# Optimization experiments

Measured on AMD Instinct MI355X. Metric: run time of the kernel, lower is better.

The kernel has to match this reference:

```python
import jax, jax.numpy as jnp
import numpy as np

N_NODES = 100000
N_EDGES = 800000
VOCAB = 100
D_FEAT = 10
D = 64
EPS = 1e-8  # torch F.cosine_similarity eps


def setup_inputs() -> dict:
    key = jax.random.key(0)
    ks = jax.random.split(key, 8)
    return {
        "nodes": jax.random.randint(ks[0], (N_NODES,), 0, VOCAB),
        "edges": jax.random.randint(ks[1], (N_EDGES, 2), 0, N_NODES),
        "features": jax.random.normal(ks[2], (N_NODES, D_FEAT), dtype=jnp.float32),
        "node_emb": jax.random.normal(ks[3], (VOCAB, D), dtype=jnp.float32),
        "feat_W": jax.random.normal(ks[4], (D, D_FEAT), dtype=jnp.float32) * 0.1,
        "feat_b": jnp.zeros((D,), dtype=jnp.float32),
        "conv1_W": jax.random.normal(ks[5], (D, D), dtype=jnp.float32) * 0.1,
        "conv1_b": jnp.zeros((D,), dtype=jnp.float32),
        "pattern_emb": jax.random.normal(ks[6], (VOCAB, D), dtype=jnp.float32),
        "pattern_id": 42,  # hash(node_type) % 100
    }


def reference(nodes, edges, features, node_emb, feat_W, feat_b,
              conv1_W, conv1_b, pattern_emb, pattern_id):
    # initial embeddings: type embedding + linear feature projection  [N, D]
    embeds = node_emb[nodes] + (features @ feat_W.T + feat_b)

    src, dst = edges[:, 0], edges[:, 1]
    for _ in range(2):  # fixed 2 message-passing rounds (structural loop)
        # scatter-add messages from src to dst (order-independent sum)
        agg = jnp.zeros_like(embeds).at[dst].add(embeds[src])
        embeds = jax.nn.relu((embeds + agg) @ conv1_W.T + conv1_b)

    # cosine similarity of each node embedding against the pattern embedding
    p = pattern_emb[pattern_id]  # [D]
    num = embeds @ p  # [N]
    denom = jnp.maximum(jnp.linalg.norm(embeds, axis=1), EPS) * \
            jnp.maximum(jnp.linalg.norm(p), EPS)
    return num / denom  # [N] match scores
```

## Files before the change

### kernel.cpp

```cpp
#include <hip/hip_runtime.h>
#include <hip/hip_bf16.h>

#define N_NODES 100000
#define N_EDGES 800000
#define D 64
#define SCAN_B 256
#define NB1 ((N_NODES + SCAN_B - 1) / SCAN_B)
#define FILL_BLOCKS (N_EDGES / 256)
#define INIT_BLOCKS (N_NODES * D / 256)
#define CT 64
#define XS 68
#define OS 72

__device__ __forceinline__ unsigned short f2bf(float f) {
    union { float f; unsigned u; } v; v.f = f;
    unsigned r = v.u + 0x7fffu + ((v.u >> 16) & 1u);
    return (unsigned short)(r >> 16);
}
__device__ __forceinline__ void acc_bf8(float acc[8], uint4 u) {
    acc[0] += __uint_as_float(u.x << 16);
    acc[1] += __uint_as_float(u.x & 0xffff0000u);
    acc[2] += __uint_as_float(u.y << 16);
    acc[3] += __uint_as_float(u.y & 0xffff0000u);
    acc[4] += __uint_as_float(u.z << 16);
    acc[5] += __uint_as_float(u.z & 0xffff0000u);
    acc[6] += __uint_as_float(u.w << 16);
    acc[7] += __uint_as_float(u.w & 0xffff0000u);
}

__global__ __launch_bounds__(256) void hist_rank_kernel(
        const int2* __restrict__ edges,
        int* __restrict__ deg,
        int* __restrict__ rank) {
    int t = blockIdx.x * 256 + threadIdx.x;
    int2 e = edges[t];
    rank[t] = atomicAdd(&deg[e.y], 1);
}

__global__ void scan1_kernel(const int* __restrict__ deg,
                             int* __restrict__ row_ptr,
                             int* __restrict__ bsum) {
    __shared__ int tmp[SCAN_B];
    int t = threadIdx.x;
    int i = blockIdx.x * SCAN_B + t;
    int v = (i < N_NODES) ? deg[i] : 0;
    tmp[t] = v;
    __syncthreads();
#pragma unroll
    for (int off = 1; off < SCAN_B; off <<= 1) {
        int a = (t >= off) ? tmp[t - off] : 0;
        __syncthreads();
        tmp[t] += a;
        __syncthreads();
    }
    if (i < N_NODES) row_ptr[i] = tmp[t] - v;
    if (t == SCAN_B - 1) bsum[blockIdx.x] = tmp[t];
}

__global__ void scan2_kernel(const int* __restrict__ bsum, int* __restrict__ boff) {
    __shared__ int tmp[512];
    int t = threadIdx.x;
    int v = (t < NB1) ? bsum[t] : 0;
    tmp[t] = v;
    __syncthreads();
#pragma unroll
    for (int off = 1; off < 512; off <<= 1) {
        int a = (t >= off) ? tmp[t - off] : 0;
        __syncthreads();
        tmp[t] += a;
        __syncthreads();
    }
    if (t < NB1) boff[t] = tmp[t] - v;
}

__global__ void scan3_kernel(int* __restrict__ row_ptr,
                             const int* __restrict__ boff) {
    int i = blockIdx.x * SCAN_B + threadIdx.x;
    if (i < N_NODES) row_ptr[i] += boff[i >> 8];
    if (i == 0) row_ptr[N_NODES] = N_EDGES;
}

__global__ __launch_bounds__(256) void fill_init_kernel(
        const int2* __restrict__ edges,
        const int* __restrict__ rank,
        const int* __restrict__ rowp,
        int* __restrict__ col,
        const int* __restrict__ nodes,
        const float* __restrict__ features,
        const float* __restrict__ node_emb,
        const float* __restrict__ feat_W,
        const float* __restrict__ feat_b,
        unsigned short* __restrict__ embeds) {
    if (blockIdx.x < FILL_BLOCKS) {
        int t = blockIdx.x * 256 + threadIdx.x;
        int2 e = edges[t];
        col[rowp[e.y] + rank[t]] = e.x;
    } else {
        int tid = (blockIdx.x - FILL_BLOCKS) * 256 + threadIdx.x;
        int node = tid >> 6;
        int d = tid & 63;
        float acc = feat_b[d];
        const float* f = features + (size_t)node * 10;
        const float* w = feat_W + (size_t)d * 10;
#pragma unroll
        for (int j = 0; j < 10; ++j) acc += f[j] * w[j];
        embeds[tid] = f2bf(node_emb[(size_t)nodes[node] * D + d] + acc);
    }
}

__global__ __launch_bounds__(256, 6) void gather_x_kernel(
        const unsigned short* __restrict__ emb_in,
        const int* __restrict__ rowp,
        const int* __restrict__ col,
        float* __restrict__ x_out) {
    int lane = threadIdx.x & 63;
    int wv   = threadIdx.x >> 6;
    int node = blockIdx.x * 4 + wv;
    int g = lane >> 3;
    int c = lane & 7;

    int start = rowp[node];
    int end   = rowp[node + 1];

    float acc[8];
#pragma unroll
    for (int j = 0; j < 8; ++j) acc[j] = 0.f;
    if (g == 0) {
        uint4 u = ((const uint4*)(emb_in + (size_t)node * D))[c];
        acc_bf8(acc, u);
    }

    for (int base = start; base < end; base += 32) {
        int nb = end - base; if (nb > 32) nb = 32;
        int idx = (lane < nb) ? col[base + lane] : 0;
#pragma unroll
        for (int r = 0; r < 4; ++r) {
            int s = r * 8 + g;
            int src = __shfl(idx, s, 64);
            if (s < nb) {
                uint4 u = ((const uint4*)(emb_in + (size_t)src * D))[c];
                acc_bf8(acc, u);
            }
        }
    }

#pragma unroll
    for (int m = 8; m <= 32; m <<= 1) {
#pragma unroll
        for (int j = 0; j < 8; ++j) acc[j] += __shfl_xor(acc[j], m, 64);
    }

    if (g == 0) {
        float4 a0 = make_float4(acc[0], acc[1], acc[2], acc[3]);
        float4 a1 = make_float4(acc[4], acc[5], acc[6], acc[7]);
        float4* o = (float4*)(x_out + (size_t)node * D);
        o[2 * c]     = a0;
        o[2 * c + 1] = a1;
    }
}

template <bool SCORE>
__global__ __launch_bounds__(256) void conv_tile_kernel(
        const float* __restrict__ x,
        const float* __restrict__ W,
        const float* __restrict__ b,
        const float* __restrict__ pattern_emb,
        const int* __restrict__ pattern_id,
        unsigned short* __restrict__ emb_out,
        float* __restrict__ score_out) {
    __shared__ float Xs[CT][XS];
    __shared__ float Wsh[D][XS];
    __shared__ unsigned short Os[CT][OS];
    __shared__ float ps[D];

    int t = threadIdx.x;
    int base = blockIdx.x * CT;
    int i = t & 15;
    int j = t >> 4;

    float bj[4];
#pragma unroll
    for (int dj = 0; dj < 4; ++dj) bj[dj] = b[j + 16 * dj];

    {
        int c = t & 15;
        int r0 = t >> 4;
#pragma unroll
        for (int p4 = 0; p4 < 4; ++p4) {
            int r = r0 + p4 * 16;
            float4 wv4 = ((const float4*)(W + (size_t)r * D))[c];
            *((float4*)&Wsh[r][4 * c]) = wv4;
            int node = base + r;
            int nc = node < N_NODES ? node : (N_NODES - 1);
            float4 xv4 = ((const float4*)(x + (size_t)nc * D))[c];
            *((float4*)&Xs[r][4 * c]) = xv4;
        }
    }
    if (SCORE && t < D) ps[t] = pattern_emb[(size_t)pattern_id[0] * D + t];
    __syncthreads();

    float acc[4][4] = {};
    for (int k4 = 0; k4 < 16; ++k4) {
        float4 xr[4], wr[4];
#pragma unroll
        for (int di = 0; di < 4; ++di) xr[di] = *((const float4*)&Xs[i + 16 * di][4 * k4]);
#pragma unroll
        for (int dj = 0; dj < 4; ++dj) wr[dj] = *((const float4*)&Wsh[j + 16 * dj][4 * k4]);
#pragma unroll
        for (int di = 0; di < 4; ++di)
#pragma unroll
            for (int dj = 0; dj < 4; ++dj)
                acc[di][dj] += xr[di].x * wr[dj].x + xr[di].y * wr[dj].y
                             + xr[di].z * wr[dj].z + xr[di].w * wr[dj].w;
    }

    if (!SCORE) {
#pragma unroll
        for (int di = 0; di < 4; ++di)
#pragma unroll
            for (int dj = 0; dj < 4; ++dj)
                Os[i + 16 * di][j + 16 * dj] = f2bf(fmaxf(acc[di][dj] + bj[dj], 0.f));
        __syncthreads();
#pragma unroll
        for (int q = 0; q < 2; ++q) {
            int idx = t + q * 256;
            int r = idx >> 3, seg = idx & 7;
            int node = base + r;
            if (node < N_NODES)
                ((uint4*)(emb_out + (size_t)node * D))[seg] = *((const uint4*)&Os[r][8 * seg]);
        }
    } else {
        __syncthreads();
#pragma unroll
        for (int di = 0; di < 4; ++di)
#pragma unroll
            for (int dj = 0; dj < 4; ++dj)
                Xs[i + 16 * di][j + 16 * dj] = fmaxf(acc[di][dj] + bj[dj], 0.f);
        __syncthreads();
        if (t < CT) {
            float dot = 0.f, n2 = 0.f, pn = 0.f;
#pragma unroll 8
            for (int k = 0; k < D; ++k) {
                float yk = Xs[t][k];
                float pk = ps[k];
                dot += yk * pk; n2 += yk * yk; pn += pk * pk;
            }
            int node = base + t;
            if (node < N_NODES)
                score_out[node] = dot / (fmaxf(sqrtf(n2), 1e-8f) * fmaxf(sqrtf(pn), 1e-8f));
        }
    }
}

__global__ void init_embeds_kernel(const int* __restrict__ nodes,
                                   const float* __restrict__ features,
                                   const float* __restrict__ node_emb,
                                   const float* __restrict__ feat_W,
                                   const float* __restrict__ feat_b,
                                   float* __restrict__ embeds) {
    int tid = blockIdx.x * blockDim.x + threadIdx.x;
    if (tid >= N_NODES * D) return;
    int node = tid >> 6;
    int d = tid & 63;
    float acc = feat_b[d];
    const float* f = features + (size_t)node * 10;
    const float* w = feat_W + (size_t)d * 10;
#pragma unroll
    for (int j = 0; j < 10; ++j) acc += f[j] * w[j];
    embeds[tid] = node_emb[(size_t)nodes[node] * D + d] + acc;
}

__global__ void scatter_add_kernel(const int* __restrict__ edges,
                                   const float* __restrict__ embeds,
                                   float* __restrict__ agg) {
    int tid = blockIdx.x * blockDim.x + threadIdx.x;
    int edge = tid >> 6;
    int lane = tid & 63;
    if (edge >= N_EDGES) return;
    int src = edges[2 * edge + 0];
    int dst = edges[2 * edge + 1];
    atomicAdd(&agg[(size_t)dst * D + lane], embeds[(size_t)src * D + lane]);
}

__global__ void conv_inplace_kernel(const float* __restrict__ agg,
                                    const float* __restrict__ W,
                                    const float* __restrict__ b,
                                    float* __restrict__ embeds) {
    __shared__ float Ws[D * 65];
    __shared__ float xs[4][D];
    for (int i = threadIdx.x; i < D * D; i += blockDim.x) {
        int d = i >> 6, k = i & 63;
        Ws[d * 65 + k] = W[i];
    }
    __syncthreads();
    int lane_d = threadIdx.x & 63;
    int local_n = threadIdx.x >> 6;
    float bias = b[lane_d];
    const int n_chunks = (N_NODES + 3) / 4;
    for (int chunk = blockIdx.x; chunk < n_chunks; chunk += gridDim.x) {
        int node = chunk * 4 + local_n;
        if (node < N_NODES) {
            size_t base = (size_t)node * D + lane_d;
            xs[local_n][lane_d] = embeds[base] + agg[base];
        }
        __syncthreads();
        if (node < N_NODES) {
            float acc = bias;
#pragma unroll
            for (int k = 0; k < D; ++k) acc += xs[local_n][k] * Ws[lane_d * 65 + k];
            embeds[(size_t)node * D + lane_d] = fmaxf(acc, 0.0f);
        }
        __syncthreads();
    }
}

__global__ void final_score_kernel(const float* __restrict__ embeds,
                                   const float* __restrict__ pattern_emb,
                                   const int* __restrict__ pattern_id,
                                   float* __restrict__ out) {
    int lane = threadIdx.x & 63;
    int wave = threadIdx.x >> 6;
    int node = blockIdx.x * 4 + wave;
    int pid = pattern_id[0];
    float p = pattern_emb[(size_t)pid * D + lane];
    float pn = p * p;
#pragma unroll
    for (int m = 32; m > 0; m >>= 1) pn += __shfl_xor(pn, m, 64);
    if (node < N_NODES) {
        float e = embeds[(size_t)node * D + lane];
        float dot = e * p;
        float n2 = e * e;
#pragma unroll
        for (int m = 32; m > 0; m >>= 1) {
            dot += __shfl_xor(dot, m, 64);
            n2  += __shfl_xor(n2, m, 64);
        }
        if (lane == 0) {
            float denom = fmaxf(sqrtf(n2), 1e-8f) * fmaxf(sqrtf(pn), 1e-8f);
            out[node] = dot / denom;
        }
    }
}

extern "C" void kernel_launch(void* const* d_in, const int* in_sizes, int n_in,
                              void* d_out, int out_size, void* d_ws, size_t ws_size,
                              hipStream_t stream) {
    const int*   nodes       = (const int*)d_in[0];
    const int*   edges       = (const int*)d_in[1];
    const float* features    = (const float*)d_in[2];
    const float* node_emb    = (const float*)d_in[3];
    const float* feat_W      = (const float*)d_in[4];
    const float* feat_b      = (const float*)d_in[5];
    const float* conv1_W     = (const float*)d_in[6];
    const float* conv1_b     = (const float*)d_in[7];
    const float* pattern_emb = (const float*)d_in[8];
    const int*   pattern_id  = (const int*)d_in[9];
    float* out = (float*)d_out;

    const size_t emb_f32_bytes = (size_t)N_NODES * D * sizeof(float);
    const size_t emb_bf_bytes  = (size_t)N_NODES * D * 2;
    auto align256 = [](size_t x) { return (x + 255) & ~(size_t)255; };

    size_t o_embA = 0;
    size_t o_embB = o_embA + align256(emb_bf_bytes);
    size_t o_xbuf = o_embB + align256(emb_bf_bytes);
    size_t o_col  = o_xbuf + align256(emb_f32_bytes);
    size_t o_rank = o_col  + align256((size_t)N_EDGES * 4);
    size_t o_row  = o_rank + align256((size_t)N_EDGES * 4);
    size_t o_deg  = o_row  + align256((size_t)(N_NODES + 1) * 4);
    size_t o_bsum = o_deg  + align256((size_t)N_NODES * 4);
    size_t o_boff = o_bsum + align256((size_t)NB1 * 4);
    size_t need   = o_boff + align256((size_t)NB1 * 4);

    char* ws = (char*)d_ws;

    if (ws_size >= need) {
        unsigned short* embA = (unsigned short*)(ws + o_embA);
        unsigned short* embB = (unsigned short*)(ws + o_embB);
        float* xbuf = (float*)(ws + o_xbuf);
        int*   col  = (int*)(ws + o_col);
        int*   rank = (int*)(ws + o_rank);
        int*   rowp = (int*)(ws + o_row);
        int*   deg  = (int*)(ws + o_deg);
        int*   bsum = (int*)(ws + o_bsum);
        int*   boff = (int*)(ws + o_boff);

        hipMemsetAsync(deg, 0, (size_t)N_NODES * 4, stream);
        hist_rank_kernel<<<FILL_BLOCKS, 256, 0, stream>>>((const int2*)edges, deg, rank);
        scan1_kernel<<<NB1, SCAN_B, 0, stream>>>(deg, rowp, bsum);
        scan2_kernel<<<1, 512, 0, stream>>>(bsum, boff);
        scan3_kernel<<<NB1, SCAN_B, 0, stream>>>(rowp, boff);
        fill_init_kernel<<<FILL_BLOCKS + INIT_BLOCKS, 256, 0, stream>>>(
            (const int2*)edges, rank, rowp, col,
            nodes, features, node_emb, feat_W, feat_b, embA);

        const int conv_grid = (N_NODES + CT - 1) / CT;

        gather_x_kernel<<<N_NODES / 4, 256, 0, stream>>>(embA, rowp, col, xbuf);
        conv_tile_kernel<false><<<conv_grid, 256, 0, stream>>>(
            xbuf, conv1_W, conv1_b, pattern_emb, pattern_id, embB, nullptr);
        gather_x_kernel<<<N_NODES / 4, 256, 0, stream>>>(embB, rowp, col, xbuf);
        conv_tile_kernel<true><<<conv_grid, 256, 0, stream>>>(
            xbuf, conv1_W, conv1_b, pattern_emb, pattern_id, nullptr, out);
    } else {
        float* embeds = (float*)ws;
        float* agg = (float*)(ws + align256(emb_f32_bytes));
        init_embeds_kernel<<<(N_NODES * D + 255) / 256, 256, 0, stream>>>(
            nodes, features, node_emb, feat_W, feat_b, embeds);
        for (int it = 0; it < 2; ++it) {
            hipMemsetAsync(agg, 0, emb_f32_bytes, stream);
            long long total = (long long)N_EDGES * 64;
            scatter_add_kernel<<<(int)((total + 255) / 256), 256, 0, stream>>>(edges, embeds, agg);
            conv_inplace_kernel<<<2048, 256, 0, stream>>>(agg, conv1_W, conv1_b, embeds);
        }
        final_score_kernel<<<(N_NODES + 3) / 4, 256, 0, stream>>>(
            embeds, pattern_emb, pattern_id, out);
    }
}
```

Before: 259.7 us.

## Merge scan passes and rewrite gather to one wave-wide row per neighbor

Replaces the separate block-sum scan and offset-add kernels with one kernel where each block reduces the preceding block sums itself, removing a launch and a serial single-block step. The gather kernel is rewritten so each of the 64 lanes reads one bf16 element of a neighbor row (128-byte row per wave per neighbor) instead of 8 lanes reading 16-byte chunks for 8 neighbors at once. This drops the cross-lane shuffle reduction and uses two accumulators, but it has fewer bytes in flight per lane and issues more load instructions per neighbor. The launch-bounds occupancy hint is also removed.

```diff
diff --git a/kernel.cpp b/kernel.cpp
--- a/kernel.cpp
+++ b/kernel.cpp
@@ -17,15 +17,8 @@
     unsigned r = v.u + 0x7fffu + ((v.u >> 16) & 1u);
     return (unsigned short)(r >> 16);
 }
-__device__ __forceinline__ void acc_bf8(float acc[8], uint4 u) {
-    acc[0] += __uint_as_float(u.x << 16);
-    acc[1] += __uint_as_float(u.x & 0xffff0000u);
-    acc[2] += __uint_as_float(u.y << 16);
-    acc[3] += __uint_as_float(u.y & 0xffff0000u);
-    acc[4] += __uint_as_float(u.z << 16);
-    acc[5] += __uint_as_float(u.z & 0xffff0000u);
-    acc[6] += __uint_as_float(u.w << 16);
-    acc[7] += __uint_as_float(u.w & 0xffff0000u);
+__device__ __forceinline__ float bf2f(unsigned short u) {
+    return __uint_as_float(((unsigned)u) << 16);
 }
 
 __global__ __launch_bounds__(256) void hist_rank_kernel(
@@ -57,26 +50,24 @@
     if (t == SCAN_B - 1) bsum[blockIdx.x] = tmp[t];
 }
 
-__global__ void scan2_kernel(const int* __restrict__ bsum, int* __restrict__ boff) {
-    __shared__ int tmp[512];
+__global__ void scan23_kernel(int* __restrict__ row_ptr,
+                              const int* __restrict__ bsum) {
+    __shared__ int red[SCAN_B];
     int t = threadIdx.x;
-    int v = (t < NB1) ? bsum[t] : 0;
-    tmp[t] = v;
+    int partial = 0;
+    if (t < blockIdx.x && t < NB1) partial += bsum[t];
+    int t2 = t + 256;
+    if (t2 < blockIdx.x && t2 < NB1) partial += bsum[t2];
+    red[t] = partial;
     __syncthreads();
 #pragma unroll
-    for (int off = 1; off < 512; off <<= 1) {
-        int a = (t >= off) ? tmp[t - off] : 0;
-        __syncthreads();
-        tmp[t] += a;
-        __syncthreads();
-    }
-    if (t < NB1) boff[t] = tmp[t] - v;
-}
-
-__global__ void scan3_kernel(int* __restrict__ row_ptr,
-                             const int* __restrict__ boff) {
-    int i = blockIdx.x * SCAN_B + threadIdx.x;
-    if (i < N_NODES) row_ptr[i] += boff[i >> 8];
+    for (int off = 128; off > 0; off >>= 1) {
+        if (t < off) red[t] += red[t + off];
+        __syncthreads();
+    }
+    int boff = red[0];
+    int i = blockIdx.x * SCAN_B + t;
+    if (i < N_NODES) row_ptr[i] += boff;
     if (i == 0) row_ptr[N_NODES] = N_EDGES;
 }
 
@@ -108,7 +99,7 @@
     }
 }
 
-__global__ __launch_bounds__(256, 6) void gather_x_kernel(
+__global__ __launch_bounds__(256) void gather_x_kernel(
         const unsigned short* __restrict__ emb_in,
         const int* __restrict__ rowp,
         const int* __restrict__ col,
@@ -116,47 +107,27 @@
     int lane = threadIdx.x & 63;
     int wv   = threadIdx.x >> 6;
     int node = blockIdx.x * 4 + wv;
-    int g = lane >> 3;
-    int c = lane & 7;
 
     int start = rowp[node];
     int end   = rowp[node + 1];
 
-    float acc[8];
-#pragma unroll
-    for (int j = 0; j < 8; ++j) acc[j] = 0.f;
-    if (g == 0) {
-        uint4 u = ((const uint4*)(emb_in + (size_t)node * D))[c];
-        acc_bf8(acc, u);
-    }
-
-    for (int base = start; base < end; base += 32) {
-        int nb = end - base; if (nb > 32) nb = 32;
-        int idx = (lane < nb) ? col[base + lane] : 0;
-#pragma unroll
-        for (int r = 0; r < 4; ++r) {
-            int s = r * 8 + g;
-            int src = __shfl(idx, s, 64);
-            if (s < nb) {
-                uint4 u = ((const uint4*)(emb_in + (size_t)src * D))[c];
-                acc_bf8(acc, u);
+    float acc0 = bf2f(emb_in[(size_t)node * D + lane]);
+    float acc1 = 0.f;
+
+    for (int base = start; base < end; base += 8) {
+        int nb = end - base; if (nb > 8) nb = 8;
+        int off = lane & 7; if (off >= nb) off = 0;
+        int idx = col[base + off];
+#pragma unroll
+        for (int r = 0; r < 8; ++r) {
+            if (r < nb) {
+                int src = __shfl(idx, r, 64);
+                float v = bf2f(emb_in[(size_t)src * D + lane]);
+                if (r & 1) acc1 += v; else acc0 += v;
             }
         }
     }
-
-#pragma unroll
-    for (int m = 8; m <= 32; m <<= 1) {
-#pragma unroll
-        for (int j = 0; j < 8; ++j) acc[j] += __shfl_xor(acc[j], m, 64);
-    }
-
-    if (g == 0) {
-        float4 a0 = make_float4(acc[0], acc[1], acc[2], acc[3]);
-        float4 a1 = make_float4(acc[4], acc[5], acc[6], acc[7]);
-        float4* o = (float4*)(x_out + (size_t)node * D);
-        o[2 * c]     = a0;
-        o[2 * c + 1] = a1;
-    }
+    x_out[(size_t)node * D + lane] = acc0 + acc1;
 }
 
 template <bool SCORE>
@@ -383,13 +354,11 @@
         int*   rowp = (int*)(ws + o_row);
         int*   deg  = (int*)(ws + o_deg);
         int*   bsum = (int*)(ws + o_bsum);
-        int*   boff = (int*)(ws + o_boff);
 
         hipMemsetAsync(deg, 0, (size_t)N_NODES * 4, stream);
         hist_rank_kernel<<<FILL_BLOCKS, 256, 0, stream>>>((const int2*)edges, deg, rank);
         scan1_kernel<<<NB1, SCAN_B, 0, stream>>>(deg, rowp, bsum);
-        scan2_kernel<<<1, 512, 0, stream>>>(bsum, boff);
-        scan3_kernel<<<NB1, SCAN_B, 0, stream>>>(rowp, boff);
+        scan23_kernel<<<NB1, SCAN_B, 0, stream>>>(rowp, bsum);
         fill_init_kernel<<<FILL_BLOCKS + INIT_BLOCKS, 256, 0, stream>>>(
             (const int2*)edges, rank, rowp, col,
             nodes, features, node_emb, feat_W, feat_b, embA);
```

Result: slower. 310.0 us (+19.4%).
